# Performance work log

Measured on AMD Instinct MI355X. Metric: run time of the kernel, lower is better.

The kernel has to match this reference:

```python
import jax, jax.numpy as jnp
import numpy as np

N, C, D = 4, 1024, 768
H, E, M, P, R = 12, 24, 4, 552, 97
OFFSET = 1  # bert offset for [CLS]


def setup_inputs() -> dict:
    key = jax.random.key(0)
    ks = jax.random.split(key, 16)
    s = 0.02
    return {
        'sequence_output': jax.random.normal(ks[0], (N, C, D), jnp.float32),
        'attention': jax.random.uniform(ks[1], (N, H, C, C), jnp.float32),
        'entity_pos': jax.random.randint(ks[2], (N, E, M), 0, C - 2),
        'hts': jax.random.randint(ks[3], (N, P, 2), 0, E),
        'rels': jax.random.normal(ks[4], (R, D), jnp.float32),
        'We': jax.random.normal(ks[5], (3 * D, D), jnp.float32) * s,
        'be': jnp.zeros((D,), jnp.float32),
        'Wq': jax.random.normal(ks[6], (D, D), jnp.float32) * s,
        'bq': jnp.zeros((D,), jnp.float32),
        'Wk': jax.random.normal(ks[7], (D, D), jnp.float32) * s,
        'bk': jnp.zeros((D,), jnp.float32),
        'Wv': jax.random.normal(ks[8], (D, D), jnp.float32) * s,
        'bv': jnp.zeros((D,), jnp.float32),
        'ln_g': jnp.ones((D,), jnp.float32),
        'ln_b': jnp.zeros((D,), jnp.float32),
        'Wc': jax.random.normal(ks[9], (D, R), jnp.float32) * s,
        'bc': jnp.zeros((R,), jnp.float32),
    }


def reference(sequence_output, attention, entity_pos, hts, rels,
              We, be, Wq, bq, Wk, bk, Wv, bv, ln_g, ln_b, Wc, bc):
    n, c, d = sequence_output.shape
    h = attention.shape[1]
    hd = d // h
    b3 = jnp.arange(n)[:, None, None]
    pos = entity_pos + OFFSET                                  # [n,E,M]
    # --- get_hrt: mention gathers + logsumexp / mean pooling ---
    ment_emb = sequence_output[b3, pos]                        # [n,E,M,d]
    ent_emb = jax.nn.logsumexp(ment_emb, axis=2)               # [n,E,d]
    ment_att = attention[b3, :, pos]                           # [n,E,M,h,c]
    ent_att = ment_att.mean(axis=2)                            # [n,E,h,c]
    hi, ti = hts[..., 0], hts[..., 1]                          # [n,P]
    b2 = jnp.arange(n)[:, None]
    hs = ent_emb[b2, hi]                                       # [n,P,d]
    ts = ent_emb[b2, ti]
    h_att = ent_att[b2, hi]                                    # [n,P,h,c]
    t_att = ent_att[b2, ti]
    ht_att = (h_att * t_att).mean(axis=2)                      # [n,P,c]
    ht_att = ht_att / (ht_att.sum(-1, keepdims=True) + 1e-5)
    rs = jnp.einsum('npc,ncd->npd', ht_att, sequence_output)   # [n,P,d]
    # --- extractor ---
    htr = jnp.tanh(jnp.concatenate([hs, ts, rs], axis=-1) @ We + be)  # [n,P,d]
    # --- double-softmax MultiHeadAttention (eval: dropout = identity) ---
    p = htr.shape[1]
    q = (htr @ Wq + bq).reshape(n, p, h, hd).transpose(2, 0, 1, 3)    # [h,n,P,hd]
    k = (rels @ Wk + bk).reshape(-1, h, hd).transpose(1, 0, 2)        # [h,R,hd]
    v = (rels @ Wv + bv).reshape(-1, h, hd).transpose(1, 0, 2)
    inv_sqrt_d = 1.0 / jnp.sqrt(jnp.float32(d))
    scores = jnp.einsum('hnpe,hre->hnpr', q, k) * inv_sqrt_d
    out = jnp.einsum('hnpr,hre->hnpe', jax.nn.softmax(scores, axis=-1), v)
    scores2 = jnp.einsum('hnpe,hnqe->hnpq', out, out) * inv_sqrt_d
    out = jnp.einsum('hnpq,hnqe->hnpe', jax.nn.softmax(scores2, axis=-1), out)
    out = jnp.tanh(out.transpose(1, 2, 0, 3).reshape(n, p, d))
    # --- residual + LayerNorm + classifier ---
    x = htr + out
    mu = x.mean(-1, keepdims=True)
    var = ((x - mu) ** 2).mean(-1, keepdims=True)
    x = (x - mu) / jnp.sqrt(var + 1e-5) * ln_g + ln_b
    logits = x.reshape(n * p, d) @ Wc + bc                      # [n*P, R]
    return logits
```

## Files before the change

### kernel.cpp

```cpp
#include <hip/hip_runtime.h>
#include <hip/hip_bf16.h>

#define N_ 4
#define C_ 1024
#define D_ 768
#define H_ 12
#define E_ 24
#define M_ 4
#define P_ 552
#define R_ 97
#define HD_ 64
#define D3_ (3*D_)
#define NP_ (N_*P_)

#define SCALE_ 0.036084391824351615f

typedef __attribute__((ext_vector_type(8))) short v8s;
typedef __attribute__((ext_vector_type(4))) float v4f;

__device__ inline ushort f2bf(float x) {
    union { float f; unsigned u; } v; v.f = x;
    unsigned r = (v.u + 0x7FFF + ((v.u >> 16) & 1)) >> 16;
    return (ushort)r;
}

__device__ inline void gl_lds16(const ushort* g, ushort* l) {
    __builtin_amdgcn_global_load_lds(
        (const __attribute__((address_space(1))) unsigned int*)(const void*)g,
        (__attribute__((address_space(3))) unsigned int*)(void*)l,
        16, 0, 0);
}

__device__ inline void tcast32(const float* __restrict__ X, ushort* __restrict__ Xt,
                               int K, int N, int yt, int xt, float (*tile)[33], int t) {
    int row = t >> 5, col = t & 31;
    int r0 = yt * 32, c0 = xt * 32;
    #pragma unroll
    for (int i = 0; i < 4; i++) {
        int r = r0 + row + i*8, c = c0 + col;
        tile[row + i*8][col] = (r < K && c < N) ? X[(long)r*N + c] : 0.f;
    }
    __syncthreads();
    #pragma unroll
    for (int i = 0; i < 4; i++) {
        int n = c0 + row + i*8, k = r0 + col;
        if (n < N && k < K) Xt[(long)n*K + k] = f2bf(tile[col][row + i*8]);
    }
}

__global__ __launch_bounds__(256) void k_prep(
        const float* __restrict__ seq, const float* __restrict__ We,
        const float* __restrict__ Wq, const float* __restrict__ Wk,
        const float* __restrict__ Wv, const float* __restrict__ Wc,
        const float* __restrict__ rels,
        ushort* __restrict__ seqT, ushort* __restrict__ WeT, ushort* __restrict__ W3T,
        ushort* __restrict__ WcT, ushort* __restrict__ relsB) {
    __shared__ float tile[32][33];
    int b = blockIdx.x, t = threadIdx.x;
    if (b < 3072) {
        int z = b / 768, r = b % 768;
        tcast32(seq + (long)z*C_*D_, seqT + (long)z*D_*C_, C_, D_, r/24, r%24, tile, t);
    } else if (b < 4800) {
        int r = b - 3072;
        tcast32(We, WeT, D3_, D_, r/24, r%24, tile, t);
    } else if (b < 6528) {
        int r3 = b - 4800;
        int z = r3 / 576, r = r3 % 576;
        const float* X = (z == 0) ? Wq : (z == 1) ? Wk : Wv;
        tcast32(X, W3T + (size_t)z*D_*D_, D_, D_, r/24, r%24, tile, t);
    } else if (b < 6624) {
        int r = b - 6528;
        tcast32(Wc, WcT, D_, R_, r/4, r%4, tile, t);
    } else {
        int base = (b - 6624) * 1024 + t * 4;
        #pragma unroll
        for (int j = 0; j < 4; j++) {
            int i = base + j;
            if (i < R_*D_) relsB[i] = f2bf(rels[i]);
        }
    }
}

__global__ void k_ent(const float* __restrict__ seq, const float* __restrict__ att,
                      const int* __restrict__ epos,
                      float* __restrict__ entEmb, float* __restrict__ entAtt) {
    int b = blockIdx.x, t = threadIdx.x;
    if (b < 288) {
        int idx = b*256 + t;
        int d  = idx % D_;
        int ne = idx / D_;
        int e  = ne % E_;
        int n  = ne / E_;
        const int* pp = epos + (n*E_ + e)*M_;
        float v[M_];
        float mx = -1e30f;
        #pragma unroll
        for (int m = 0; m < M_; m++) {
            int pos = pp[m] + 1;
            v[m] = seq[((long)n*C_ + pos)*D_ + d];
            mx = fmaxf(mx, v[m]);
        }
        float s = 0.f;
        #pragma unroll
        for (int m = 0; m < M_; m++) s += expf(v[m] - mx);
        entEmb[idx] = mx + logf(s);
    } else {
        long idx = (long)(b - 288)*256 + t;
        int c = idx % C_;
        long r = idx / C_;
        int h = r % H_; r /= H_;
        int e = r % E_;
        int n = r / E_;
        const int* pp = epos + (n*E_ + e)*M_;
        float s = 0.f;
        #pragma unroll
        for (int m = 0; m < M_; m++) {
            int pos = pp[m] + 1;
            s += att[(((long)n*H_ + h)*C_ + pos)*C_ + c];
        }
        entAtt[idx] = s * (1.0f / M_);
    }
}

__global__ void k_gath(const float* __restrict__ entEmb, const float* __restrict__ entAtt,
                       const int* __restrict__ hts,
                       ushort* __restrict__ bcat, ushort* __restrict__ bhtAtt) {
    __shared__ float red[256];
    int b = blockIdx.x, t = threadIdx.x;
    if (b < 6624) {
        int idx = b*256 + t;
        int d  = idx % D_;
        int np = idx / D_;
        int p  = np % P_;
        int n  = np / P_;
        int hi = hts[(n*P_ + p)*2 + 0];
        int ti = hts[(n*P_ + p)*2 + 1];
        bcat[(long)np*D3_ + d]       = f2bf(entEmb[((long)n*E_ + hi)*D_ + d]);
        bcat[(long)np*D3_ + D_ + d]  = f2bf(entEmb[((long)n*E_ + ti)*D_ + d]);
    } else {
        int np = b - 6624;
        int p = np % P_, n = np / P_;
        int hi = hts[(n*P_ + p)*2 + 0];
        int ti = hts[(n*P_ + p)*2 + 1];
        const float* ha = entAtt + ((long)n*E_ + hi)*H_*C_;
        const float* ta = entAtt + ((long)n*E_ + ti)*H_*C_;
        float vals[C_/256];
        float lsum = 0.f;
        #pragma unroll
        for (int i = 0; i < C_/256; i++) {
            int c = t + i*256;
            float s = 0.f;
            #pragma unroll
            for (int h = 0; h < H_; h++) s += ha[h*C_ + c] * ta[h*C_ + c];
            s *= (1.0f / H_);
            vals[i] = s;
            lsum += s;
        }
        red[t] = lsum; __syncthreads();
        for (int s1 = 128; s1; s1 >>= 1) { if (t < s1) red[t] += red[t+s1]; __syncthreads(); }
        float inv = 1.0f / (red[0] + 1e-5f);
        #pragma unroll
        for (int i = 0; i < C_/256; i++)
            bhtAtt[(long)np*C_ + t + i*256] = f2bf(vals[i] * inv);
    }
}

__global__ __launch_bounds__(256) void k_mfma_bt(
        const ushort* __restrict__ A, const ushort* __restrict__ Bt,
        const float* __restrict__ bias, float* __restrict__ Cf, ushort* __restrict__ Cb,
        int M, int N, int Npad, int K,
        int lda, int ldb, int ldcf, int ldcb, int nb2,
        long sA1, long sA2, long sB1, long sB2,
        long sCf1, long sCf2, long sCb1, long sCb2,
        int act, int biasM) {
    int z = blockIdx.z;
    int b1 = z / nb2, b2 = z % nb2;
    A  += b1*sA1 + b2*sA2;
    Bt += b1*sB1 + b2*sB2;
    long cfo = b1*sCf1 + b2*sCf2;
    long cbo = b1*sCb1 + b2*sCb2;
    __shared__ ushort As[2][128*32];
    __shared__ ushort Bs[2][128*32];
    int t = threadIdx.x;
    int m0 = blockIdx.y * 128, n0 = blockIdx.x * 128;
    int lr = t >> 2;
    int lc = (t & 3) * 8;
    int wv = t >> 6, lane = t & 63;
    int quad = lane >> 4, lm = lane & 15;
    int wm = (wv >> 1) * 64, wn = (wv & 1) * 64;

    const ushort* pA0 = A + (long)min(m0 + lr,      M-1)*lda + lc;
    const ushort* pA1 = A + (long)min(m0 + lr + 64, M-1)*lda + lc;
    const ushort* pB0 = Bt + (long)min(n0 + lr,      N-1)*ldb + lc;
    const ushort* pB1 = Bt + (long)min(n0 + lr + 64, N-1)*ldb + lc;

    v4f acc[4][4];
    #pragma unroll
    for (int i = 0; i < 4; i++)
        #pragma unroll
        for (int j = 0; j < 4; j++)
            acc[i][j] = (v4f){0.f, 0.f, 0.f, 0.f};

    gl_lds16(pA0, &As[0][t*8]);
    gl_lds16(pA1, &As[0][2048 + t*8]);
    gl_lds16(pB0, &Bs[0][t*8]);
    gl_lds16(pB1, &Bs[0][2048 + t*8]);

    int cur = 0;
    for (int k0 = 0; k0 < K; k0 += 32) {
        __syncthreads();
        if (k0 + 32 < K) {
            int nb = cur ^ 1;
            gl_lds16(pA0 + k0 + 32, &As[nb][t*8]);
            gl_lds16(pA1 + k0 + 32, &As[nb][2048 + t*8]);
            gl_lds16(pB0 + k0 + 32, &Bs[nb][t*8]);
            gl_lds16(pB1 + k0 + 32, &Bs[nb][2048 + t*8]);
        }
        v8s a[4], b[4];
        #pragma unroll
        for (int i = 0; i < 4; i++)
            a[i] = *(const v8s*)(&As[cur][(wm + i*16 + lm)*32 + quad*8]);
        #pragma unroll
        for (int j = 0; j < 4; j++)
            b[j] = *(const v8s*)(&Bs[cur][(wn + j*16 + lm)*32 + quad*8]);
        #pragma unroll
        for (int i = 0; i < 4; i++)
            #pragma unroll
            for (int j = 0; j < 4; j++)
                acc[i][j] = __builtin_amdgcn_mfma_f32_16x16x32_bf16(a[i], b[j], acc[i][j], 0, 0, 0);
        cur ^= 1;
    }

    #pragma unroll
    for (int j = 0; j < 4; j++) {
        int gn = n0 + wn + j*16 + lm;
        if (gn >= Npad) continue;
        bool vld = gn < N;
        float bvn = (bias && !biasM && vld) ? bias[gn] : 0.f;
        #pragma unroll
        for (int i = 0; i < 4; i++) {
            #pragma unroll
            for (int reg = 0; reg < 4; reg++) {
                int gm = m0 + wm + i*16 + quad*4 + reg;
                if (gm >= M) continue;
                float v = 0.f;
                if (vld) {
                    v = acc[i][j][reg] + bvn;
                    if (bias && biasM) v += bias[gm];
                    if (act == 1) v = tanhf(v);
                }
                if (Cf) Cf[cfo + (long)gm*ldcf + gn] = v;
                if (Cb) Cb[cbo + (long)gm*ldcb + gn] = f2bf(v);
            }
        }
    }
}

__global__ __launch_bounds__(256) void k_attn1f(
        const ushort* __restrict__ qb, const ushort* __restrict__ kb,
        const ushort* __restrict__ vT, ushort* __restrict__ o1b, ushort* __restrict__ o1T) {
    int mt = blockIdx.x, h = blockIdx.y;
    int m0 = mt * 128;
    __shared__ ushort U[128*128];
    __shared__ ushort Vs[64*128];
    __shared__ float rowm[2][128];
    __shared__ float rowl[2][128];
    ushort* Qs = U;
    ushort* Ks = U + 128*64;
    ushort* Ps = U;
    int t = threadIdx.x;
    const uint4 z4 = {0u,0u,0u,0u};
    #pragma unroll
    for (int i = 0; i < 4; i++) {
        int id = t + i*256;
        int row = id >> 3, c8 = (id & 7) * 8;
        int np = m0 + row;
        uint4 qv = z4;
        if (np < NP_) qv = *(const uint4*)(qb + (long)np*D_ + h*HD_ + c8);
        *(uint4*)(Qs + row*64 + c8) = qv;
        uint4 kv = z4;
        if (row < R_) kv = *(const uint4*)(kb + (long)row*D_ + h*HD_ + c8);
        *(uint4*)(Ks + row*64 + c8) = kv;
    }
    #pragma unroll
    for (int i = 0; i < 4; i++) {
        int id = t + i*256;
        int e = id >> 4, c8 = (id & 15) * 8;
        *(uint4*)(Vs + e*128 + c8) = *(const uint4*)(vT + ((long)h*HD_ + e)*128 + c8);
    }
    __syncthreads();
    int wv = t >> 6, lane = t & 63;
    int quad = lane >> 4, lm = lane & 15;
    int wm = (wv >> 1) * 64, wn = (wv & 1) * 64;
    int side = wv & 1;

    v4f acc[4][4];
    #pragma unroll
    for (int i = 0; i < 4; i++)
        #pragma unroll
        for (int j = 0; j < 4; j++)
            acc[i][j] = (v4f){0.f,0.f,0.f,0.f};
    #pragma unroll
    for (int k0 = 0; k0 < 64; k0 += 32) {
        v8s a[4], b[4];
        #pragma unroll
        for (int i = 0; i < 4; i++) a[i] = *(const v8s*)(Qs + (wm + i*16 + lm)*64 + k0 + quad*8);
        #pragma unroll
        for (int j = 0; j < 4; j++) b[j] = *(const v8s*)(Ks + (wn + j*16 + lm)*64 + k0 + quad*8);
        #pragma unroll
        for (int i = 0; i < 4; i++)
            #pragma unroll
            for (int j = 0; j < 4; j++)
                acc[i][j] = __builtin_amdgcn_mfma_f32_16x16x32_bf16(a[i], b[j], acc[i][j], 0, 0, 0);
    }
    #pragma unroll
    for (int j = 0; j < 4; j++) {
        int col = wn + j*16 + lm;
        bool ok = col < R_;
        #pragma unroll
        for (int i = 0; i < 4; i++)
            #pragma unroll
            for (int reg = 0; reg < 4; reg++)
                acc[i][j][reg] = ok ? acc[i][j][reg]*SCALE_ : -1e30f;
    }
    #pragma unroll
    for (int i = 0; i < 4; i++)
        #pragma unroll
        for (int reg = 0; reg < 4; reg++) {
            float m = fmaxf(fmaxf(acc[i][0][reg], acc[i][1][reg]),
                            fmaxf(acc[i][2][reg], acc[i][3][reg]));
            #pragma unroll
            for (int o = 1; o < 16; o <<= 1) m = fmaxf(m, __shfl_xor(m, o));
            if (lm == 0) rowm[side][wm + i*16 + quad*4 + reg] = m;
        }
    __syncthreads();
    #pragma unroll
    for (int i = 0; i < 4; i++)
        #pragma unroll
        for (int reg = 0; reg < 4; reg++) {
            int r = wm + i*16 + quad*4 + reg;
            float m = fmaxf(rowm[0][r], rowm[1][r]);
            float s = 0.f;
            #pragma unroll
            for (int j = 0; j < 4; j++) {
                float e = expf(acc[i][j][reg] - m);
                acc[i][j][reg] = e;
                s += e;
            }
            #pragma unroll
            for (int o = 1; o < 16; o <<= 1) s += __shfl_xor(s, o);
            if (lm == 0) rowl[side][r] = s;
        }
    __syncthreads();
    #pragma unroll
    for (int i = 0; i < 4; i++)
        #pragma unroll
        for (int reg = 0; reg < 4; reg++) {
            int r = wm + i*16 + quad*4 + reg;
            float inv = 1.0f / (rowl[0][r] + rowl[1][r]);
            #pragma unroll
            for (int j = 0; j < 4; j++)
                Ps[r*128 + wn + j*16 + lm] = f2bf(acc[i][j][reg] * inv);
        }
    __syncthreads();
    v4f acc2[2][4];
    #pragma unroll
    for (int i = 0; i < 2; i++)
        #pragma unroll
        for (int j = 0; j < 4; j++)
            acc2[i][j] = (v4f){0.f,0.f,0.f,0.f};
    int wm2 = wv * 32;
    #pragma unroll
    for (int k0 = 0; k0 < 128; k0 += 32) {
        v8s a2[2], b2[4];
        #pragma unroll
        for (int i = 0; i < 2; i++) a2[i] = *(const v8s*)(Ps + (wm2 + i*16 + lm)*128 + k0 + quad*8);
        #pragma unroll
        for (int j = 0; j < 4; j++) b2[j] = *(const v8s*)(Vs + (j*16 + lm)*128 + k0 + quad*8);
        #pragma unroll
        for (int i = 0; i < 2; i++)
            #pragma unroll
            for (int j = 0; j < 4; j++)
                acc2[i][j] = __builtin_amdgcn_mfma_f32_16x16x32_bf16(a2[i], b2[j], acc2[i][j], 0, 0, 0);
    }
    #pragma unroll
    for (int i = 0; i < 2; i++)
        #pragma unroll
        for (int j = 0; j < 4; j++)
            #pragma unroll
            for (int reg = 0; reg < 4; reg++) {
                int row = m0 + wm2 + i*16 + quad*4 + reg;
                if (row >= NP_) continue;
                int e = j*16 + lm;
                ushort bvv = f2bf(acc2[i][j][reg]);
                o1b[(long)row*D_ + h*HD_ + e] = bvv;
                int n = row / P_;
                int q = row - n*P_;
                o1T[(((long)(n*H_ + h))*HD_ + e)*576 + q] = bvv;
            }
}

__global__ __launch_bounds__(256) void k_attn2f(
        const ushort* __restrict__ o1b, const ushort* __restrict__ o1T, float* __restrict__ o2) {
    int qt = blockIdx.x;
    int zz = blockIdx.y;
    int n = zz / H_, h = zz % H_;
    int q0 = qt * 128;
    __shared__ ushort Qs[128*64];
    __shared__ ushort KV[128*64];
    __shared__ ushort Ps[128*128];
    __shared__ float rowm[2][128], rowl[2][128];
    __shared__ float mrun[128], lrun[128], alphaS[128];
    int t = threadIdx.x;
    const ushort* base = o1b + (long)n*P_*D_ + h*HD_;
    const uint4 z4 = {0u,0u,0u,0u};
    #pragma unroll
    for (int i = 0; i < 4; i++) {
        int id = t + i*256;
        int row = id >> 3, c8 = (id & 7) * 8;
        int q = q0 + row;
        uint4 v = z4;
        if (q < P_) v = *(const uint4*)(base + (long)q*D_ + c8);
        *(uint4*)(Qs + row*64 + c8) = v;
    }
    if (t < 128) { mrun[t] = -1e30f; lrun[t] = 0.f; }
    __syncthreads();
    int wv = t >> 6, lane = t & 63;
    int quad = lane >> 4, lm = lane & 15;
    int wm = (wv >> 1) * 64, wn = (wv & 1) * 64;
    int side = wv & 1;
    int wm2 = wv * 32;
    v4f acc2[2][4];
    #pragma unroll
    for (int i = 0; i < 2; i++)
        #pragma unroll
        for (int j = 0; j < 4; j++)
            acc2[i][j] = (v4f){0.f,0.f,0.f,0.f};

    for (int c = 0; c < 5; c++) {
        #pragma unroll
        for (int i = 0; i < 4; i++) {
            int id = t + i*256;
            int row = id >> 3, c8 = (id & 7) * 8;
            int q = c*128 + row;
            uint4 v = z4;
            if (q < P_) v = *(const uint4*)(base + (long)q*D_ + c8);
            *(uint4*)(KV + row*64 + c8) = v;
        }
        __syncthreads();
        v4f acc[4][4];
        #pragma unroll
        for (int i = 0; i < 4; i++)
            #pragma unroll
            for (int j = 0; j < 4; j++)
                acc[i][j] = (v4f){0.f,0.f,0.f,0.f};
        #pragma unroll
        for (int k0 = 0; k0 < 64; k0 += 32) {
            v8s a[4], b[4];
            #pragma unroll
            for (int i = 0; i < 4; i++) a[i] = *(const v8s*)(Qs + (wm + i*16 + lm)*64 + k0 + quad*8);
            #pragma unroll
            for (int j = 0; j < 4; j++) b[j] = *(const v8s*)(KV + (wn + j*16 + lm)*64 + k0 + quad*8);
            #pragma unroll
            for (int i = 0; i < 4; i++)
                #pragma unroll
                for (int j = 0; j < 4; j++)
                    acc[i][j] = __builtin_amdgcn_mfma_f32_16x16x32_bf16(a[i], b[j], acc[i][j], 0, 0, 0);
        }
        #pragma unroll
        for (int j = 0; j < 4; j++) {
            int col = c*128 + wn + j*16 + lm;
            bool ok = col < P_;
            #pragma unroll
            for (int i = 0; i < 4; i++)
                #pragma unroll
                for (int reg = 0; reg < 4; reg++)
                    acc[i][j][reg] = ok ? acc[i][j][reg]*SCALE_ : -1e30f;
        }
        #pragma unroll
        for (int i = 0; i < 4; i++)
            #pragma unroll
            for (int reg = 0; reg < 4; reg++) {
                float m = fmaxf(fmaxf(acc[i][0][reg], acc[i][1][reg]),
                                fmaxf(acc[i][2][reg], acc[i][3][reg]));
                #pragma unroll
                for (int o = 1; o < 16; o <<= 1) m = fmaxf(m, __shfl_xor(m, o));
                if (lm == 0) rowm[side][wm + i*16 + quad*4 + reg] = m;
            }
        __syncthreads();
        #pragma unroll
        for (int i = 0; i < 4; i++)
            #pragma unroll
            for (int reg = 0; reg < 4; reg++) {
                int r = wm + i*16 + quad*4 + reg;
                float mc = fmaxf(rowm[0][r], rowm[1][r]);
                float mn = fmaxf(mrun[r], mc);
                float s = 0.f;
                #pragma unroll
                for (int j = 0; j < 4; j++) {
                    float e = expf(acc[i][j][reg] - mn);
                    acc[i][j][reg] = e;
                    s += e;
                }
                #pragma unroll
                for (int o = 1; o < 16; o <<= 1) s += __shfl_xor(s, o);
                if (lm == 0) rowl[side][r] = s;
            }
        __syncthreads();
        if (side == 0 && lm == 0) {
            #pragma unroll
            for (int i = 0; i < 4; i++)
                #pragma unroll
                for (int reg = 0; reg < 4; reg++) {
                    int r = wm + i*16 + quad*4 + reg;
                    float mo = mrun[r];
                    float mc = fmaxf(rowm[0][r], rowm[1][r]);
                    float mn = fmaxf(mo, mc);
                    float al = expf(mo - mn);
                    lrun[r] = lrun[r]*al + rowl[0][r] + rowl[1][r];
                    mrun[r] = mn;
                    alphaS[r] = al;
                }
        }
        #pragma unroll
        for (int i = 0; i < 4; i++) {
            int id = t + i*256;
            int e = id >> 4, c8 = (id & 15) * 8;
            uint4 v = z4;
            if (c*128 + c8 < P_) v = *(const uint4*)(o1T + ((long)zz*HD_ + e)*576 + c*128 + c8);
            *(uint4*)(KV + e*128 + c8) = v;
        }
        #pragma unroll
        for (int i = 0; i < 4; i++)
            #pragma unroll
            for (int reg = 0; reg < 4; reg++) {
                int r = wm + i*16 + quad*4 + reg;
                #pragma unroll
                for (int j = 0; j < 4; j++)
                    Ps[r*128 + wn + j*16 + lm] = f2bf(acc[i][j][reg]);
            }
        __syncthreads();
        #pragma unroll
        for (int i = 0; i < 2; i++) {
            #pragma unroll
            for (int reg = 0; reg < 4; reg++) {
                float al = alphaS[wm2 + i*16 + quad*4 + reg];
                #pragma unroll
                for (int j = 0; j < 4; j++)
                    acc2[i][j][reg] *= al;
            }
        }
        #pragma unroll
        for (int k0 = 0; k0 < 128; k0 += 32) {
            v8s a2[2], b2[4];
            #pragma unroll
            for (int i = 0; i < 2; i++) a2[i] = *(const v8s*)(Ps + (wm2 + i*16 + lm)*128 + k0 + quad*8);
            #pragma unroll
            for (int j = 0; j < 4; j++) b2[j] = *(const v8s*)(KV + (j*16 + lm)*128 + k0 + quad*8);
            #pragma unroll
            for (int i = 0; i < 2; i++)
                #pragma unroll
                for (int j = 0; j < 4; j++)
                    acc2[i][j] = __builtin_amdgcn_mfma_f32_16x16x32_bf16(a2[i], b2[j], acc2[i][j], 0, 0, 0);
        }
        __syncthreads();
    }
    #pragma unroll
    for (int i = 0; i < 2; i++)
        #pragma unroll
        for (int j = 0; j < 4; j++)
            #pragma unroll
            for (int reg = 0; reg < 4; reg++) {
                int row = wm2 + i*16 + quad*4 + reg;
                int q = q0 + row;
                if (q >= P_) continue;
                float l = lrun[row];
                o2[((long)n*P_ + q)*D_ + h*HD_ + j*16 + lm] = acc2[i][j][reg] / l;
            }
}

__global__ void k_ln(const float* __restrict__ htr, const float* __restrict__ o2,
                     const float* __restrict__ g, const float* __restrict__ b,
                     ushort* __restrict__ bx) {
    int np = blockIdx.x;
    int t = threadIdx.x;
    __shared__ float red[256];
    float v[D_/256];
    float s = 0.f;
    #pragma unroll
    for (int i = 0; i < D_/256; i++) {
        int d = t + i*256;
        float val = htr[(long)np*D_ + d] + tanhf(o2[(long)np*D_ + d]);
        v[i] = val; s += val;
    }
    red[t] = s; __syncthreads();
    for (int s1 = 128; s1; s1 >>= 1) { if (t < s1) red[t] += red[t+s1]; __syncthreads(); }
    float mu = red[0] * (1.0f/D_);
    __syncthreads();
    float s2 = 0.f;
    #pragma unroll
    for (int i = 0; i < D_/256; i++) { float dx = v[i]-mu; s2 += dx*dx; }
    red[t] = s2; __syncthreads();
    for (int s1 = 128; s1; s1 >>= 1) { if (t < s1) red[t] += red[t+s1]; __syncthreads(); }
    float inv = rsqrtf(red[0]*(1.0f/D_) + 1e-5f);
    #pragma unroll
    for (int i = 0; i < D_/256; i++) {
        int d = t + i*256;
        bx[(long)np*D_ + d] = f2bf((v[i]-mu)*inv*g[d] + b[d]);
    }
}

extern "C" void kernel_launch(void* const* d_in, const int* in_sizes, int n_in,
                              void* d_out, int out_size, void* d_ws, size_t ws_size,
                              hipStream_t stream) {
    const float* seq   = (const float*)d_in[0];
    const float* att   = (const float*)d_in[1];
    const int*   epos  = (const int*)d_in[2];
    const int*   hts   = (const int*)d_in[3];
    const float* rels  = (const float*)d_in[4];
    const float* We    = (const float*)d_in[5];
    const float* be    = (const float*)d_in[6];
    const float* Wq    = (const float*)d_in[7];
    const float* bq    = (const float*)d_in[8];
    const float* Wk    = (const float*)d_in[9];
    const float* bk    = (const float*)d_in[10];
    const float* Wv    = (const float*)d_in[11];
    const float* bv    = (const float*)d_in[12];
    const float* ln_g  = (const float*)d_in[13];
    const float* ln_b  = (const float*)d_in[14];
    const float* Wc    = (const float*)d_in[15];
    const float* bc    = (const float*)d_in[16];
    float* out = (float*)d_out;
    float* w = (float*)d_ws;

    const int NP = NP_;

    float* entEmb  = w;
    float* entAtt  = entEmb  + (size_t)N_*E_*D_;
    float* htr     = entAtt  + (size_t)N_*E_*H_*C_;
    float* o2      = htr     + (size_t)NP*D_;
    ushort* bhtAtt = (ushort*)(o2 + (size_t)NP*D_);
    ushort* bcat   = bhtAtt + (size_t)NP*C_;
    ushort* seqT   = bcat  + (size_t)NP*D3_;
    ushort* WeT    = seqT  + (size_t)N_*D_*C_;
    ushort* WqT    = WeT   + (size_t)D_*D3_;
    ushort* WkT    = WqT   + (size_t)D_*D_;
    ushort* WvT    = WkT   + (size_t)D_*D_;
    ushort* WcT    = WvT   + (size_t)D_*D_;
    ushort* relsB  = WcT   + (size_t)D_*R_;
    ushort* bhtr   = relsB + (size_t)R_*D_;
    ushort* bqb    = bhtr  + (size_t)NP*D_;
    ushort* bkb    = bqb   + (size_t)NP*D_;
    ushort* vT     = bkb   + (size_t)R_*D_;
    ushort* o1b    = vT    + (size_t)D_*128;
    ushort* o1T    = o1b   + (size_t)NP*D_;
    ushort* bxb    = o1T   + (size_t)48*HD_*576;

    k_prep<<<6697, 256, 0, stream>>>(seq, We, Wq, Wk, Wv, Wc, rels,
                                     seqT, WeT, WqT, WcT, relsB);
    k_ent<<<4896, 256, 0, stream>>>(seq, att, epos, entEmb, entAtt);
    k_gath<<<8832, 256, 0, stream>>>(entEmb, entAtt, hts, bcat, bhtAtt);

    k_mfma_bt<<<dim3(6, 5, N_), 256, 0, stream>>>(
        bhtAtt, seqT, nullptr, nullptr, bcat + 2*D_,
        P_, D_, D_, C_, C_, C_, 0, D3_, 1,
        (long)P_*C_, 0, (long)D_*C_, 0, 0, 0, (long)P_*D3_, 0, 0, 0);

    k_mfma_bt<<<dim3(6, 18, 1), 256, 0, stream>>>(
        bcat, WeT, be, htr, bhtr,
        NP, D_, D_, D3_, D3_, D3_, D_, D_, 1,
        0, 0, 0, 0, 0, 0, 0, 0, 1, 0);

    k_mfma_bt<<<dim3(6, 18, 1), 256, 0, stream>>>(
        bhtr, WqT, bq, nullptr, bqb,
        NP, D_, D_, D_, D_, D_, 0, D_, 1,
        0, 0, 0, 0, 0, 0, 0, 0, 0, 0);

    k_mfma_bt<<<dim3(6, 1, 1), 256, 0, stream>>>(
        relsB, WkT, bk, nullptr, bkb,
        R_, D_, D_, D_, D_, D_, 0, D_, 1,
        0, 0, 0, 0, 0, 0, 0, 0, 0, 0);

    k_mfma_bt<<<dim3(1, 6, 1), 256, 0, stream>>>(
        WvT, relsB, bv, nullptr, vT,
        D_, R_, 128, D_, D_, D_, 0, 128, 1,
        0, 0, 0, 0, 0, 0, 0, 0, 0, 1);

    k_attn1f<<<dim3(18, 12), 256, 0, stream>>>(bqb, bkb, vT, o1b, o1T);

    k_attn2f<<<dim3(5, 48), 256, 0, stream>>>(o1b, o1T, o2);

    k_ln<<<NP, 256, 0, stream>>>(htr, o2, ln_g, ln_b, bxb);

    k_mfma_bt<<<dim3(1, 18, 1), 256, 0, stream>>>(
        bxb, WcT, bc, out, nullptr,
        NP, R_, R_, D_, D_, D_, R_, 0, 1,
        0, 0, 0, 0, 0, 0, 0, 0, 0, 0);
}
```

Baseline: 614.1 us.

## Deepen GEMM LDS pipeline, merge QKV GEMMs, drop transposed o1 buffer

The shared GEMM core moves from a 2-stage to a 4-slot LDS ring with prefetch distance 2, using explicit vmcnt waits and a single barrier per iteration to hide global-load latency. The Q, K and V projection GEMMs are merged into one launch to cut launch overhead and idle tail blocks. The attention-1 kernel no longer writes a transposed copy of its output. Attention-2 instead transposes the V tile into LDS itself and parallelises the running-softmax update across 128 threads. The trade-offs are doubled LDS per GEMM block, which may lower occupancy, and scattered 2-byte LDS stores in the transpose.

After: 544.3 us. 11.4% less time.

```diff
diff --git a/kernel.cpp b/kernel.cpp
--- a/kernel.cpp
+++ b/kernel.cpp
@@ -165,24 +165,17 @@
     }
 }
 
-__global__ __launch_bounds__(256) void k_mfma_bt(
+__device__ __forceinline__ void gemm_core(
+        int bx, int by,
         const ushort* __restrict__ A, const ushort* __restrict__ Bt,
         const float* __restrict__ bias, float* __restrict__ Cf, ushort* __restrict__ Cb,
+        long cfo, long cbo,
         int M, int N, int Npad, int K,
-        int lda, int ldb, int ldcf, int ldcb, int nb2,
-        long sA1, long sA2, long sB1, long sB2,
-        long sCf1, long sCf2, long sCb1, long sCb2,
-        int act, int biasM) {
-    int z = blockIdx.z;
-    int b1 = z / nb2, b2 = z % nb2;
-    A  += b1*sA1 + b2*sA2;
-    Bt += b1*sB1 + b2*sB2;
-    long cfo = b1*sCf1 + b2*sCf2;
-    long cbo = b1*sCb1 + b2*sCb2;
-    __shared__ ushort As[2][128*32];
-    __shared__ ushort Bs[2][128*32];
+        int lda, int ldb, int ldcf, int ldcb,
+        int act, int biasM,
+        ushort* __restrict__ As, ushort* __restrict__ Bs) {
     int t = threadIdx.x;
-    int m0 = blockIdx.y * 128, n0 = blockIdx.x * 128;
+    int m0 = by * 128, n0 = bx * 128;
     int lr = t >> 2;
     int lc = (t & 3) * 8;
     int wv = t >> 6, lane = t & 63;
@@ -201,34 +194,43 @@
         for (int j = 0; j < 4; j++)
             acc[i][j] = (v4f){0.f, 0.f, 0.f, 0.f};
 
-    gl_lds16(pA0, &As[0][t*8]);
-    gl_lds16(pA1, &As[0][2048 + t*8]);
-    gl_lds16(pB0, &Bs[0][t*8]);
-    gl_lds16(pB1, &Bs[0][2048 + t*8]);
-
-    int cur = 0;
-    for (int k0 = 0; k0 < K; k0 += 32) {
-        __syncthreads();
-        if (k0 + 32 < K) {
-            int nb = cur ^ 1;
-            gl_lds16(pA0 + k0 + 32, &As[nb][t*8]);
-            gl_lds16(pA1 + k0 + 32, &As[nb][2048 + t*8]);
-            gl_lds16(pB0 + k0 + 32, &Bs[nb][t*8]);
-            gl_lds16(pB1 + k0 + 32, &Bs[nb][2048 + t*8]);
+    int nIter = K >> 5;
+    gl_lds16(pA0, As + t*8);
+    gl_lds16(pA1, As + 2048 + t*8);
+    gl_lds16(pB0, Bs + t*8);
+    gl_lds16(pB1, Bs + 2048 + t*8);
+    if (nIter > 1) {
+        gl_lds16(pA0 + 32, As + 4096 + t*8);
+        gl_lds16(pA1 + 32, As + 4096 + 2048 + t*8);
+        gl_lds16(pB0 + 32, Bs + 4096 + t*8);
+        gl_lds16(pB1 + 32, Bs + 4096 + 2048 + t*8);
+    }
+
+    for (int it = 0; it < nIter; ++it) {
+        int cur = (it & 3) * 4096;
+        if (it + 2 < nIter) {
+            asm volatile("s_waitcnt vmcnt(4)\n\ts_barrier" ::: "memory");
+            int nb = ((it + 2) & 3) * 4096;
+            int k2 = (it + 2) << 5;
+            gl_lds16(pA0 + k2, As + nb + t*8);
+            gl_lds16(pA1 + k2, As + nb + 2048 + t*8);
+            gl_lds16(pB0 + k2, Bs + nb + t*8);
+            gl_lds16(pB1 + k2, Bs + nb + 2048 + t*8);
+        } else {
+            asm volatile("s_waitcnt vmcnt(0)\n\ts_barrier" ::: "memory");
         }
         v8s a[4], b[4];
         #pragma unroll
         for (int i = 0; i < 4; i++)
-            a[i] = *(const v8s*)(&As[cur][(wm + i*16 + lm)*32 + quad*8]);
+            a[i] = *(const v8s*)(As + cur + (wm + i*16 + lm)*32 + quad*8);
         #pragma unroll
         for (int j = 0; j < 4; j++)
-            b[j] = *(const v8s*)(&Bs[cur][(wn + j*16 + lm)*32 + quad*8]);
+            b[j] = *(const v8s*)(Bs + cur + (wn + j*16 + lm)*32 + quad*8);
         #pragma unroll
         for (int i = 0; i < 4; i++)
             #pragma unroll
             for (int j = 0; j < 4; j++)
                 acc[i][j] = __builtin_amdgcn_mfma_f32_16x16x32_bf16(a[i], b[j], acc[i][j], 0, 0, 0);
-        cur ^= 1;
     }
 
     #pragma unroll
@@ -256,9 +258,50 @@
     }
 }
 
+__global__ __launch_bounds__(256) void k_mfma_bt(
+        const ushort* __restrict__ A, const ushort* __restrict__ Bt,
+        const float* __restrict__ bias, float* __restrict__ Cf, ushort* __restrict__ Cb,
+        int M, int N, int Npad, int K,
+        int lda, int ldb, int ldcf, int ldcb, int nb2,
+        long sA1, long sA2, long sB1, long sB2,
+        long sCf1, long sCf2, long sCb1, long sCb2,
+        int act, int biasM) {
+    __shared__ ushort As[4][128*32];
+    __shared__ ushort Bs[4][128*32];
+    int z = blockIdx.z;
+    int b1 = z / nb2, b2 = z % nb2;
+    gemm_core(blockIdx.x, blockIdx.y,
+              A + b1*sA1 + b2*sA2, Bt + b1*sB1 + b2*sB2, bias, Cf, Cb,
+              b1*sCf1 + b2*sCf2, b1*sCb1 + b2*sCb2,
+              M, N, Npad, K, lda, ldb, ldcf, ldcb, act, biasM,
+              &As[0][0], &Bs[0][0]);
+}
+
+__global__ __launch_bounds__(256) void k_qkv(
+        const ushort* __restrict__ bhtr, const ushort* __restrict__ WqT,
+        const ushort* __restrict__ WkT, const ushort* __restrict__ WvT,
+        const ushort* __restrict__ relsB,
+        const float* __restrict__ bq, const float* __restrict__ bk,
+        const float* __restrict__ bv,
+        ushort* __restrict__ bqb, ushort* __restrict__ bkb, ushort* __restrict__ vT) {
+    __shared__ ushort As[4][128*32];
+    __shared__ ushort Bs[4][128*32];
+    int x = blockIdx.x, y = blockIdx.y;
+    if (y < 18) {
+        gemm_core(x, y, bhtr, WqT, bq, nullptr, bqb, 0, 0,
+                  NP_, D_, D_, D_, D_, D_, 0, D_, 0, 0, &As[0][0], &Bs[0][0]);
+    } else if (y == 18) {
+        gemm_core(x, 0, relsB, WkT, bk, nullptr, bkb, 0, 0,
+                  R_, D_, D_, D_, D_, D_, 0, D_, 0, 0, &As[0][0], &Bs[0][0]);
+    } else if (x == 0) {
+        gemm_core(0, y - 19, WvT, relsB, bv, nullptr, vT, 0, 0,
+                  D_, R_, 128, D_, D_, D_, 0, 128, 0, 1, &As[0][0], &Bs[0][0]);
+    }
+}
+
 __global__ __launch_bounds__(256) void k_attn1f(
         const ushort* __restrict__ qb, const ushort* __restrict__ kb,
-        const ushort* __restrict__ vT, ushort* __restrict__ o1b, ushort* __restrict__ o1T) {
+        const ushort* __restrict__ vT, ushort* __restrict__ o1b) {
     int mt = blockIdx.x, h = blockIdx.y;
     int m0 = mt * 128;
     __shared__ ushort U[128*128];
@@ -391,17 +434,12 @@
             for (int reg = 0; reg < 4; reg++) {
                 int row = m0 + wm2 + i*16 + quad*4 + reg;
                 if (row >= NP_) continue;
-                int e = j*16 + lm;
-                ushort bvv = f2bf(acc2[i][j][reg]);
-                o1b[(long)row*D_ + h*HD_ + e] = bvv;
-                int n = row / P_;
-                int q = row - n*P_;
-                o1T[(((long)(n*H_ + h))*HD_ + e)*576 + q] = bvv;
+                o1b[(long)row*D_ + h*HD_ + j*16 + lm] = f2bf(acc2[i][j][reg]);
             }
 }
 
 __global__ __launch_bounds__(256) void k_attn2f(
-        const ushort* __restrict__ o1b, const ushort* __restrict__ o1T, float* __restrict__ o2) {
+        const ushort* __restrict__ o1b, float* __restrict__ o2) {
     int qt = blockIdx.x;
     int zz = blockIdx.y;
     int n = zz / H_, h = zz % H_;
@@ -507,28 +545,25 @@
                 if (lm == 0) rowl[side][r] = s;
             }
         __syncthreads();
-        if (side == 0 && lm == 0) {
-            #pragma unroll
-            for (int i = 0; i < 4; i++)
-                #pragma unroll
-                for (int reg = 0; reg < 4; reg++) {
-                    int r = wm + i*16 + quad*4 + reg;
-                    float mo = mrun[r];
-                    float mc = fmaxf(rowm[0][r], rowm[1][r]);
-                    float mn = fmaxf(mo, mc);
-                    float al = expf(mo - mn);
-                    lrun[r] = lrun[r]*al + rowl[0][r] + rowl[1][r];
-                    mrun[r] = mn;
-                    alphaS[r] = al;
-                }
+        if (t < 128) {
+            float mo = mrun[t];
+            float mc = fmaxf(rowm[0][t], rowm[1][t]);
+            float mn = fmaxf(mo, mc);
+            float al = expf(mo - mn);
+            lrun[t] = lrun[t]*al + rowl[0][t] + rowl[1][t];
+            mrun[t] = mn;
+            alphaS[t] = al;
         }
         #pragma unroll
         for (int i = 0; i < 4; i++) {
             int id = t + i*256;
-            int e = id >> 4, c8 = (id & 15) * 8;
+            int q = id & 127, e0 = (id >> 7) * 8;
+            int gq = c*128 + q;
             uint4 v = z4;
-            if (c*128 + c8 < P_) v = *(const uint4*)(o1T + ((long)zz*HD_ + e)*576 + c*128 + c8);
-            *(uint4*)(KV + e*128 + c8) = v;
+            if (gq < P_) v = *(const uint4*)(base + (long)gq*D_ + e0);
+            const ushort* pv = (const ushort*)&v;
+            #pragma unroll
+            for (int j = 0; j < 8; j++) KV[(e0+j)*128 + q] = pv[j];
         }
         #pragma unroll
         for (int i = 0; i < 4; i++)
@@ -653,8 +688,7 @@
     ushort* bkb    = bqb   + (size_t)NP*D_;
     ushort* vT     = bkb   + (size_t)R_*D_;
     ushort* o1b    = vT    + (size_t)D_*128;
-    ushort* o1T    = o1b   + (size_t)NP*D_;
-    ushort* bxb    = o1T   + (size_t)48*HD_*576;
+    ushort* bxb    = o1b   + (size_t)NP*D_;
 
     k_prep<<<6697, 256, 0, stream>>>(seq, We, Wq, Wk, Wv, Wc, rels,
                                      seqT, WeT, WqT, WcT, relsB);
@@ -671,24 +705,12 @@
         NP, D_, D_, D3_, D3_, D3_, D_, D_, 1,
         0, 0, 0, 0, 0, 0, 0, 0, 1, 0);
 
-    k_mfma_bt<<<dim3(6, 18, 1), 256, 0, stream>>>(
-        bhtr, WqT, bq, nullptr, bqb,
-        NP, D_, D_, D_, D_, D_, 0, D_, 1,
-        0, 0, 0, 0, 0, 0, 0, 0, 0, 0);
-
-    k_mfma_bt<<<dim3(6, 1, 1), 256, 0, stream>>>(
-        relsB, WkT, bk, nullptr, bkb,
-        R_, D_, D_, D_, D_, D_, 0, D_, 1,
-        0, 0, 0, 0, 0, 0, 0, 0, 0, 0);
-
-    k_mfma_bt<<<dim3(1, 6, 1), 256, 0, stream>>>(
-        WvT, relsB, bv, nullptr, vT,
-        D_, R_, 128, D_, D_, D_, 0, 128, 1,
-        0, 0, 0, 0, 0, 0, 0, 0, 0, 1);
-
-    k_attn1f<<<dim3(18, 12), 256, 0, stream>>>(bqb, bkb, vT, o1b, o1T);
-
-    k_attn2f<<<dim3(5, 48), 256, 0, stream>>>(o1b, o1T, o2);
+    k_qkv<<<dim3(6, 25, 1), 256, 0, stream>>>(
+        bhtr, WqT, WkT, WvT, relsB, bq, bk, bv, bqb, bkb, vT);
+
+    k_attn1f<<<dim3(18, 12), 256, 0, stream>>>(bqb, bkb, vT, o1b);
+
+    k_attn2f<<<dim3(5, 48), 256, 0, stream>>>(o1b, o2);
 
     k_ln<<<NP, 256, 0, stream>>>(htr, o2, ln_g, ln_b, bxb);
 
```
